# Optimization experiments

Hardware: AMD Instinct MI355X
Metric: run time of the kernel (lower is better)

The kernel has to match this reference:

```python
import jax, jax.numpy as jnp
import numpy as np

EMBED_DIM = 1024
NUM_HEADS = 16
NUM_SIGNALS = 2
B, N = 2, 1024


def taylor_kernel(x):
    # phi(x) = [1, x, (x (outer) x)/sqrt(2)] over the last dim
    d = x.shape[-1]
    x2 = (x[..., :, None] * x[..., None, :]).reshape(*x.shape[:-1], d * d) / 2 ** 0.5
    ones = jnp.ones((*x.shape[:-1], 1), dtype=x.dtype)
    return jnp.concatenate([ones, x, x2], axis=-1)


def setup_inputs() -> dict:
    key = jax.random.key(0)
    ks = jax.random.split(key, 11)
    C = EMBED_DIM
    inp = {
        'query': jax.random.normal(ks[0], (B, N, C), dtype=jnp.float32),
        'key':   jax.random.normal(ks[1], (B, N, C), dtype=jnp.float32),
        'value': jax.random.normal(ks[2], (B, N, C), dtype=jnp.float32),
        'Wq': jax.random.normal(ks[3], (C, C), dtype=jnp.float32) * 0.02,
        'bq': jnp.zeros((C,), dtype=jnp.float32),
        'Wk': jax.random.normal(ks[4], (C, C), dtype=jnp.float32) * 0.02,
        'bk': jnp.zeros((C,), dtype=jnp.float32),
        'Wv': jax.random.normal(ks[5], (C, C), dtype=jnp.float32) * 0.02,
        'bv': jnp.zeros((C,), dtype=jnp.float32),
        'Wo': jax.random.normal(ks[6], (C, C), dtype=jnp.float32) * 0.02,
        'bo': jnp.zeros((C,), dtype=jnp.float32),
    }
    return inp


def reference(query, key, value, Wq, bq, Wk, bk, Wv, bv, Wo, bo):
    Bsz, Nq, C = query.shape
    M = key.shape[1]
    H, S = NUM_HEADS, NUM_SIGNALS
    hd = C // H          # head_dim
    sd = hd // S         # signal_dim
    scale = sd ** -0.5

    q = (query @ Wq.T + bq).reshape(Bsz, Nq, H, S, sd).transpose(0, 2, 3, 1, 4)  # (B,H,S,N,sd)
    k = (key   @ Wk.T + bk).reshape(Bsz, M,  H, S, sd).transpose(0, 2, 3, 1, 4)  # (B,H,S,M,sd)
    v = (value @ Wv.T + bv).reshape(Bsz, M,  H, hd).transpose(0, 2, 1, 3)        # (B,H,M,hd)

    q_phi = taylor_kernel(q * scale)   # (B,H,S,N,F), F = 1+sd+sd^2
    k_phi = taylor_kernel(k)           # (B,H,S,M,F)

    # KV aggregation: O(M * F * hd) per (b,h,s); v broadcast over signal dim
    kv = jnp.einsum('bhsmf,bhmd->bhsfd', k_phi, v)           # (B,H,S,F,hd)
    numer = jnp.einsum('bhsnf,bhsfd->bhsnd', q_phi, kv)      # (B,H,S,N,hd)
    k_sum = k_phi.sum(axis=-2)                               # (B,H,S,F)
    denom = jnp.einsum('bhsnf,bhsf->bhsn', q_phi, k_sum)[..., None]

    out = (numer / (denom + 1e-6)).mean(axis=2)              # avg over signals -> (B,H,N,hd)
    out = out.transpose(0, 2, 1, 3).reshape(Bsz, Nq, C)
    return out @ Wo.T + bo
```

## Files before the change

### kernel.cpp

```cpp
#include <hip/hip_runtime.h>
#include <hip/hip_bf16.h>

#define CC 1024
#define NN 1024
#define BB 2
#define HH 16
#define NT (NN / 64)
#define QSCALE 0.17677669529663687f

typedef short bf16x8 __attribute__((ext_vector_type(8)));
typedef float f32x4  __attribute__((ext_vector_type(4)));
typedef unsigned int u32x2 __attribute__((ext_vector_type(2)));

__device__ __forceinline__ f32x4 mfma16(bf16x8 a, bf16x8 b, f32x4 c) {
    return __builtin_amdgcn_mfma_f32_16x16x32_bf16(a, b, c, 0, 0, 0);
}
__device__ __forceinline__ short f2bf(float x) {
    __hip_bfloat16 h = __float2bfloat16(x);
    return *reinterpret_cast<short*>(&h);
}
__device__ __forceinline__ float bf2f(short s) {
    __hip_bfloat16 h;
    *reinterpret_cast<short*>(&h) = s;
    return __bfloat162float(h);
}
__device__ __forceinline__ int xcd_logical(int hw, int nwg) {
    return (hw & 7) * (nwg >> 3) + (hw >> 3);
}

__global__ __launch_bounds__(256) void qkv_proj(
    const float* __restrict__ xq, const float* __restrict__ xk, const float* __restrict__ xv,
    const float* __restrict__ wq, const float* __restrict__ wk, const float* __restrict__ wv,
    const float* __restrict__ bq, const float* __restrict__ bk, const float* __restrict__ bv,
    short* __restrict__ qt, short* __restrict__ kt, short* __restrict__ vt)
{
    __shared__ short LD[18432];
    short (*A)[72]  = (short(*)[72])LD;
    short (*Bt)[72] = (short(*)[72])(LD + 128 * 72);
    short (*T)[136] = (short(*)[136])LD;

    const int L = xcd_logical(blockIdx.x, 384);
    const int z = L >> 7;
    const int rem = L & 127;
    const int row0 = (rem >> 3) * 128;
    const int col0 = (rem & 7) * 128;

    const int tid  = threadIdx.x;
    const int lane = tid & 63, wave = tid >> 6;
    const int wr = wave >> 1, wc = wave & 1;
    const int l16 = lane & 15, lk = lane >> 4;

    const float* X    = (z == 0) ? xq : (z == 1) ? xk : xv;
    const float* W    = (z == 0) ? wq : (z == 1) ? wk : wv;
    const float* bias = (z == 0) ? bq : (z == 1) ? bk : bv;

    const int str = tid >> 4;
    const int stc = (tid & 15) << 2;

    float4 pa[8], pb[8];
#pragma unroll
    for (int p = 0; p < 8; ++p) {
        pa[p] = *(const float4*)&X[(size_t)(row0 + p * 16 + str) * CC + stc];
        pb[p] = *(const float4*)&W[(size_t)(col0 + p * 16 + str) * CC + stc];
    }

    f32x4 acc[4][4];
#pragma unroll
    for (int i = 0; i < 4; ++i)
#pragma unroll
        for (int j = 0; j < 4; ++j) acc[i][j] = (f32x4){0.f, 0.f, 0.f, 0.f};

    for (int k0 = 0; k0 < CC; k0 += 64) {
#pragma unroll
        for (int p = 0; p < 8; ++p) {
            ushort4 ua = { (unsigned short)f2bf(pa[p].x), (unsigned short)f2bf(pa[p].y),
                           (unsigned short)f2bf(pa[p].z), (unsigned short)f2bf(pa[p].w) };
            *(ushort4*)&A[p * 16 + str][stc] = ua;
            ushort4 ub = { (unsigned short)f2bf(pb[p].x), (unsigned short)f2bf(pb[p].y),
                           (unsigned short)f2bf(pb[p].z), (unsigned short)f2bf(pb[p].w) };
            *(ushort4*)&Bt[p * 16 + str][stc] = ub;
        }
        if (k0 + 64 < CC) {
#pragma unroll
            for (int p = 0; p < 8; ++p) {
                pa[p] = *(const float4*)&X[(size_t)(row0 + p * 16 + str) * CC + k0 + 64 + stc];
                pb[p] = *(const float4*)&W[(size_t)(col0 + p * 16 + str) * CC + k0 + 64 + stc];
            }
        }
        __syncthreads();
#pragma unroll
        for (int ks = 0; ks < 2; ++ks) {
            bf16x8 af[4], bw[4];
#pragma unroll
            for (int i = 0; i < 4; ++i) {
                af[i] = *(const bf16x8*)&A[wr * 64 + i * 16 + l16][ks * 32 + lk * 8];
                bw[i] = *(const bf16x8*)&Bt[wc * 64 + i * 16 + l16][ks * 32 + lk * 8];
            }
#pragma unroll
            for (int mi = 0; mi < 4; ++mi)
#pragma unroll
                for (int nf = 0; nf < 4; ++nf)
                    acc[mi][nf] = mfma16(af[mi], bw[nf], acc[mi][nf]);
        }
        __syncthreads();
    }

    if (z <= 1) {
        short* outp = (z == 0) ? qt : kt;
        const float scl = (z == 0) ? QSCALE : 1.f;
#pragma unroll
        for (int mi = 0; mi < 4; ++mi)
#pragma unroll
            for (int q = 0; q < 4; ++q) {
                const int r = row0 + wr * 64 + mi * 16 + lk * 4 + q;
                const int b = r >> 10, n = r & 1023;
#pragma unroll
                for (int nf = 0; nf < 4; ++nf) {
                    const int o = col0 + wc * 64 + nf * 16 + l16;
                    const int h = o >> 6, s = (o >> 5) & 1, ii = o & 31;
                    float y = (acc[mi][nf][q] + bias[o]) * scl;
                    outp[(((size_t)((b * HH + h) * 2 + s)) << 15) + n * 32 + ii] = f2bf(y);
                }
            }
    } else {
#pragma unroll
        for (int mi = 0; mi < 4; ++mi)
#pragma unroll
            for (int nf = 0; nf < 4; ++nf)
#pragma unroll
                for (int q = 0; q < 4; ++q) {
                    const int c = wc * 64 + nf * 16 + l16;
                    const int r = wr * 64 + mi * 16 + lk * 4 + q;
                    T[c][r] = f2bf(acc[mi][nf][q] + bias[col0 + c]);
                }
        __syncthreads();
        const int b  = row0 >> 10, n0 = row0 & 1023;
        const int c  = tid >> 1, half = tid & 1;
        const int oc = col0 + c, h = oc >> 6, d = oc & 63;
        const size_t base = (((size_t)(b * HH + h)) * 64 + d) * NN + n0 + half * 64;
#pragma unroll
        for (int u = 0; u < 8; ++u)
            *(uint4*)&vt[base + u * 8] = *(const uint4*)&T[c][half * 64 + u * 8];
    }
}

__global__ __launch_bounds__(512) void attn_mfma(
    const short* __restrict__ qt, const short* __restrict__ kt,
    const short* __restrict__ vtg, short* __restrict__ aoh, short* __restrict__ aol)
{
    __shared__ __align__(16) short LDS_[17408];
    short* KsB = LDS_;
    short* VtB = LDS_ + 5120;
    float* OsB = (float*)LDS_;

#define KS(ss, r, c)  KsB[((ss) * 64 + (r)) * 40 + (c)]
#define VT(d, m)      VtB[(d) * 72 + (m)]
#define OS(n, d)      OsB[(n) * 68 + (d)]

    const int L = xcd_logical(blockIdx.x, 256);
    const int bh = L >> 3;
    const int n0 = (L & 7) * 128;

    const int tid  = threadIdx.x;
    const int lane = tid & 63;
    const int wid  = tid >> 6;
    const int s  = wid >> 2;
    const int hq = wid & 3;
    const int l16 = lane & 15, lk = lane >> 4;

    bf16x8 qf[2];
#pragma unroll
    for (int nf = 0; nf < 2; ++nf)
        qf[nf] = *(const bf16x8*)&qt[((size_t)(bh * 2 + s) * NN + n0 + hq * 32 + nf * 16 + l16) * 32 + lk * 8];

    const int kss = tid >> 8, kj = tid & 255, kr = kj >> 2, kc8 = (kj & 3) << 3;
    const int vd = tid >> 3, vc8 = (tid & 7) << 3;

    uint4 kpf, vpf;
    auto load_tiles = [&](int m0) {
        kpf = *(const uint4*)&kt[((size_t)(bh * 2 + kss) * NN + m0 + kr) * 32 + kc8];
        vpf = *(const uint4*)&vtg[((size_t)(bh * 64 + vd)) * NN + m0 + vc8];
    };
    auto commit_tiles = [&]() {
        *(uint4*)&KS(kss, kr, kc8) = kpf;
        *(uint4*)&VT(vd, vc8) = vpf;
    };

    f32x4 accn[2][4];
#pragma unroll
    for (int nf = 0; nf < 2; ++nf)
#pragma unroll
        for (int df = 0; df < 4; ++df) accn[nf][df] = (f32x4){0.f, 0.f, 0.f, 0.f};
    float den[2] = {0.f, 0.f};

    load_tiles(0);

    for (int t = 0; t < NT; ++t) {
        commit_tiles();
        if (t + 1 < NT) load_tiles((t + 1) * 64);
        __syncthreads();

        bf16x8 kf[4], vf[2][4];
#pragma unroll
        for (int mf = 0; mf < 4; ++mf)
            kf[mf] = *(const bf16x8*)&KS(s, mf * 16 + l16, lk * 8);
#pragma unroll
        for (int kb = 0; kb < 2; ++kb)
#pragma unroll
            for (int df = 0; df < 4; ++df)
                vf[kb][df] = *(const bf16x8*)&VT(df * 16 + l16, kb * 32 + lk * 8);

#pragma unroll
        for (int nf = 0; nf < 2; ++nf) {
            unsigned c01[4], c23[4];
#pragma unroll
            for (int mf = 0; mf < 4; ++mf) {
                f32x4 st = mfma16(kf[mf], qf[nf], (f32x4){0.f, 0.f, 0.f, 0.f});
                float p0 = 1.f + st[0] * (1.f + 0.5f * st[0]);
                float p1 = 1.f + st[1] * (1.f + 0.5f * st[1]);
                float p2 = 1.f + st[2] * (1.f + 0.5f * st[2]);
                float p3 = 1.f + st[3] * (1.f + 0.5f * st[3]);
                den[nf] += (p0 + p1) + (p2 + p3);
                asm("v_cvt_pk_bf16_f32 %0, %1, %2" : "=v"(c01[mf]) : "v"(p0), "v"(p1));
                asm("v_cvt_pk_bf16_f32 %0, %1, %2" : "=v"(c23[mf]) : "v"(p2), "v"(p3));
            }
#pragma unroll
            for (int kb = 0; kb < 2; ++kb) {
                u32x2 x0 = __builtin_amdgcn_permlane32_swap(c01[2 * kb], c01[2 * kb + 1], 0, 0);
                u32x2 w02 = __builtin_amdgcn_permlane16_swap(x0.x, x0.y, 0, 0);
                u32x2 x1 = __builtin_amdgcn_permlane32_swap(c23[2 * kb], c23[2 * kb + 1], 0, 0);
                u32x2 w13 = __builtin_amdgcn_permlane16_swap(x1.x, x1.y, 0, 0);
                uint4 u = {w02.x, w13.x, w02.y, w13.y};
                bf16x8 pf = *(bf16x8*)&u;
#pragma unroll
                for (int df = 0; df < 4; ++df)
                    accn[nf][df] = mfma16(pf, vf[kb][df], accn[nf][df]);
            }
        }
        __syncthreads();
    }

    float invq[2][4];
#pragma unroll
    for (int nf = 0; nf < 2; ++nf) {
        float d = den[nf];
        d += __shfl_xor(d, 16, 64);
        d += __shfl_xor(d, 32, 64);
#pragma unroll
        for (int q = 0; q < 4; ++q)
            invq[nf][q] = 0.5f / (__shfl(d, (lane & 48) + lk * 4 + q, 64) + 1e-6f);
    }

    if (s == 0) {
#pragma unroll
        for (int nf = 0; nf < 2; ++nf)
#pragma unroll
            for (int q = 0; q < 4; ++q)
#pragma unroll
                for (int df = 0; df < 4; ++df)
                    OS(hq * 32 + nf * 16 + lk * 4 + q, df * 16 + l16) =
                        accn[nf][df][q] * invq[nf][q];
    }
    __syncthreads();
    if (s == 1) {
        const int b = bh >> 4, h = bh & 15;
#pragma unroll
        for (int nf = 0; nf < 2; ++nf)
#pragma unroll
            for (int q = 0; q < 4; ++q) {
                const int n = hq * 32 + nf * 16 + lk * 4 + q;
#pragma unroll
                for (int df = 0; df < 4; ++df) {
                    const int d = df * 16 + l16;
                    float o = OS(n, d) + accn[nf][df][q] * invq[nf][q];
                    size_t addr = ((size_t)b * NN + n0 + n) * CC + h * 64 + d;
                    short hi = f2bf(o);
                    aoh[addr] = hi;
                    aol[addr] = f2bf(o - bf2f(hi));
                }
            }
    }
#undef KS
#undef VT
#undef OS
}

__global__ __launch_bounds__(256) void wo_proj(
    const short* __restrict__ aoh, const short* __restrict__ aol,
    const float* __restrict__ Wo, const float* __restrict__ bo,
    float* __restrict__ outp)
{
    __shared__ short Ah[64][40], Al[64][40], Wh[64][40], Wl[64][40];

    const int L = xcd_logical(blockIdx.x, 512);
    const int row0 = (L >> 4) * 64;
    const int col0 = (L & 15) * 64;

    const int tid  = threadIdx.x;
    const int lane = tid & 63, wave = tid >> 6;
    const int wr = wave >> 1, wc = wave & 1;
    const int l16 = lane & 15, lk = lane >> 4;

    const int ar  = tid >> 2, ac8 = (tid & 3) << 3;
    const int wrr = tid >> 3, wc4 = (tid & 7) << 2;

    uint4 ph, pl;
    float4 pw[2];
    ph = *(const uint4*)&aoh[(size_t)(row0 + ar) * CC + ac8];
    pl = *(const uint4*)&aol[(size_t)(row0 + ar) * CC + ac8];
#pragma unroll
    for (int p = 0; p < 2; ++p)
        pw[p] = *(const float4*)&Wo[(size_t)(col0 + p * 32 + wrr) * CC + wc4];

    f32x4 acc[2][2];
#pragma unroll
    for (int i = 0; i < 2; ++i)
#pragma unroll
        for (int j = 0; j < 2; ++j) acc[i][j] = (f32x4){0.f, 0.f, 0.f, 0.f};

    for (int k0 = 0; k0 < CC; k0 += 32) {
        *(uint4*)&Ah[ar][ac8] = ph;
        *(uint4*)&Al[ar][ac8] = pl;
#pragma unroll
        for (int p = 0; p < 2; ++p) {
            float v[4] = {pw[p].x, pw[p].y, pw[p].z, pw[p].w};
            unsigned short hs[4], ls[4];
#pragma unroll
            for (int j = 0; j < 4; ++j) {
                short hv = f2bf(v[j]);
                hs[j] = (unsigned short)hv;
                ls[j] = (unsigned short)f2bf(v[j] - bf2f(hv));
            }
            *(ushort4*)&Wh[p * 32 + wrr][wc4] = (ushort4){hs[0], hs[1], hs[2], hs[3]};
            *(ushort4*)&Wl[p * 32 + wrr][wc4] = (ushort4){ls[0], ls[1], ls[2], ls[3]};
        }
        if (k0 + 32 < CC) {
            ph = *(const uint4*)&aoh[(size_t)(row0 + ar) * CC + k0 + 32 + ac8];
            pl = *(const uint4*)&aol[(size_t)(row0 + ar) * CC + k0 + 32 + ac8];
#pragma unroll
            for (int p = 0; p < 2; ++p)
                pw[p] = *(const float4*)&Wo[(size_t)(col0 + p * 32 + wrr) * CC + k0 + 32 + wc4];
        }
        __syncthreads();
        bf16x8 ah[2], al[2], wh[2], wl[2];
#pragma unroll
        for (int i = 0; i < 2; ++i) {
            ah[i] = *(const bf16x8*)&Ah[wr * 32 + i * 16 + l16][lk * 8];
            al[i] = *(const bf16x8*)&Al[wr * 32 + i * 16 + l16][lk * 8];
            wh[i] = *(const bf16x8*)&Wh[wc * 32 + i * 16 + l16][lk * 8];
            wl[i] = *(const bf16x8*)&Wl[wc * 32 + i * 16 + l16][lk * 8];
        }
#pragma unroll
        for (int mi = 0; mi < 2; ++mi)
#pragma unroll
            for (int nj = 0; nj < 2; ++nj) {
                acc[mi][nj] = mfma16(ah[mi], wh[nj], acc[mi][nj]);
                acc[mi][nj] = mfma16(ah[mi], wl[nj], acc[mi][nj]);
                acc[mi][nj] = mfma16(al[mi], wh[nj], acc[mi][nj]);
            }
        __syncthreads();
    }

#pragma unroll
    for (int mi = 0; mi < 2; ++mi)
#pragma unroll
        for (int q = 0; q < 4; ++q) {
            const int r = row0 + wr * 32 + mi * 16 + lk * 4 + q;
#pragma unroll
            for (int nj = 0; nj < 2; ++nj) {
                const int o = col0 + wc * 32 + nj * 16 + l16;
                outp[(size_t)r * CC + o] = acc[mi][nj][q] + bo[o];
            }
        }
}

extern "C" void kernel_launch(void* const* d_in, const int* in_sizes, int n_in,
                              void* d_out, int out_size, void* d_ws, size_t ws_size,
                              hipStream_t stream) {
    const float* query = (const float*)d_in[0];
    const float* key_  = (const float*)d_in[1];
    const float* value = (const float*)d_in[2];
    const float* Wq = (const float*)d_in[3];
    const float* bq = (const float*)d_in[4];
    const float* Wk = (const float*)d_in[5];
    const float* bk = (const float*)d_in[6];
    const float* Wv = (const float*)d_in[7];
    const float* bv = (const float*)d_in[8];
    const float* Wo = (const float*)d_in[9];
    const float* bo = (const float*)d_in[10];
    float* out = (float*)d_out;

    short* qt  = (short*)d_ws;
    short* kt  = qt  + ((size_t)1 << 21);
    short* vt  = kt  + ((size_t)1 << 21);
    short* aoh = vt  + ((size_t)1 << 21);
    short* aol = aoh + ((size_t)1 << 21);

    dim3 blk(256);
    qkv_proj<<<dim3(384), blk, 0, stream>>>(query, key_, value, Wq, Wk, Wv,
                                            bq, bk, bv, qt, kt, vt);
    attn_mfma<<<dim3(256), dim3(512), 0, stream>>>(qt, kt, vt, aoh, aol);
    wo_proj<<<dim3(512), blk, 0, stream>>>(aoh, aol, Wo, bo, out);
}
```

Measured before the change: 83.33 us.

## Pre-convert QKV inputs and weights to bf16 in a separate pass

Adds a cvt_pass kernel that converts the query/key/value activations and the Wq/Wk/Wv weights from fp32 to bf16 in the workspace. The projection GEMM then loads bf16 directly, which halves its global load bytes, drops the per-tile conversion work from the inner loop, and double-buffers two 64-wide K slices held in registers. The cost is an extra kernel launch plus an extra write and read of roughly 36 MB of converted data, so the net gain depends on whether the GEMM was bound by loads or conversion.

```diff
diff --git a/kernel.cpp b/kernel.cpp
--- a/kernel.cpp
+++ b/kernel.cpp
@@ -28,9 +28,34 @@
     return (hw & 7) * (nwg >> 3) + (hw >> 3);
 }
 
-__global__ __launch_bounds__(256) void qkv_proj(
+__global__ __launch_bounds__(256) void cvt_pass(
     const float* __restrict__ xq, const float* __restrict__ xk, const float* __restrict__ xv,
     const float* __restrict__ wq, const float* __restrict__ wk, const float* __restrict__ wv,
+    short* __restrict__ xqb, short* __restrict__ xkb, short* __restrict__ xvb,
+    short* __restrict__ wqb, short* __restrict__ wkb, short* __restrict__ wvb)
+{
+    const int z = blockIdx.z;
+    const float* src = (z == 0) ? xq : (z == 1) ? xk : (z == 2) ? xv :
+                       (z == 3) ? wq : (z == 4) ? wk : wv;
+    short* dst = (z == 0) ? xqb : (z == 1) ? xkb : (z == 2) ? xvb :
+                 (z == 3) ? wqb : (z == 4) ? wkb : wvb;
+    const size_t n = (z < 3) ? ((size_t)1 << 21) : ((size_t)1 << 20);
+
+    for (size_t i = ((size_t)blockIdx.x * 256 + threadIdx.x) * 8; i < n;
+         i += (size_t)gridDim.x * 256 * 8) {
+        float4 v0 = *(const float4*)&src[i];
+        float4 v1 = *(const float4*)&src[i + 4];
+        float v[8] = {v0.x, v0.y, v0.z, v0.w, v1.x, v1.y, v1.z, v1.w};
+        unsigned short h[8];
+#pragma unroll
+        for (int j = 0; j < 8; ++j) h[j] = (unsigned short)f2bf(v[j]);
+        *(uint4*)&dst[i] = *(uint4*)h;
+    }
+}
+
+__global__ __launch_bounds__(256) void qkv_proj(
+    const short* __restrict__ xqb, const short* __restrict__ xkb, const short* __restrict__ xvb,
+    const short* __restrict__ wqb, const short* __restrict__ wkb, const short* __restrict__ wvb,
     const float* __restrict__ bq, const float* __restrict__ bk, const float* __restrict__ bv,
     short* __restrict__ qt, short* __restrict__ kt, short* __restrict__ vt)
 {
@@ -50,18 +75,20 @@
     const int wr = wave >> 1, wc = wave & 1;
     const int l16 = lane & 15, lk = lane >> 4;
 
-    const float* X    = (z == 0) ? xq : (z == 1) ? xk : xv;
-    const float* W    = (z == 0) ? wq : (z == 1) ? wk : wv;
+    const short* X    = (z == 0) ? xqb : (z == 1) ? xkb : xvb;
+    const short* W    = (z == 0) ? wqb : (z == 1) ? wkb : wvb;
     const float* bias = (z == 0) ? bq : (z == 1) ? bk : bv;
 
-    const int str = tid >> 4;
-    const int stc = (tid & 15) << 2;
-
-    float4 pa[8], pb[8];
-#pragma unroll
-    for (int p = 0; p < 8; ++p) {
-        pa[p] = *(const float4*)&X[(size_t)(row0 + p * 16 + str) * CC + stc];
-        pb[p] = *(const float4*)&W[(size_t)(col0 + p * 16 + str) * CC + stc];
+    const int srow = tid >> 3;
+    const int sc8  = (tid & 7) << 3;
+
+    uint4 pa0[4], pb0[4], pa1[4], pb1[4];
+#pragma unroll
+    for (int p = 0; p < 4; ++p) {
+        pa0[p] = *(const uint4*)&X[(size_t)(row0 + p * 32 + srow) * CC + sc8];
+        pb0[p] = *(const uint4*)&W[(size_t)(col0 + p * 32 + srow) * CC + sc8];
+        pa1[p] = *(const uint4*)&X[(size_t)(row0 + p * 32 + srow) * CC + 64 + sc8];
+        pb1[p] = *(const uint4*)&W[(size_t)(col0 + p * 32 + srow) * CC + 64 + sc8];
     }
 
     f32x4 acc[4][4];
@@ -70,21 +97,46 @@
 #pragma unroll
         for (int j = 0; j < 4; ++j) acc[i][j] = (f32x4){0.f, 0.f, 0.f, 0.f};
 
-    for (int k0 = 0; k0 < CC; k0 += 64) {
-#pragma unroll
-        for (int p = 0; p < 8; ++p) {
-            ushort4 ua = { (unsigned short)f2bf(pa[p].x), (unsigned short)f2bf(pa[p].y),
-                           (unsigned short)f2bf(pa[p].z), (unsigned short)f2bf(pa[p].w) };
-            *(ushort4*)&A[p * 16 + str][stc] = ua;
-            ushort4 ub = { (unsigned short)f2bf(pb[p].x), (unsigned short)f2bf(pb[p].y),
-                           (unsigned short)f2bf(pb[p].z), (unsigned short)f2bf(pb[p].w) };
-            *(ushort4*)&Bt[p * 16 + str][stc] = ub;
-        }
-        if (k0 + 64 < CC) {
-#pragma unroll
-            for (int p = 0; p < 8; ++p) {
-                pa[p] = *(const float4*)&X[(size_t)(row0 + p * 16 + str) * CC + k0 + 64 + stc];
-                pb[p] = *(const float4*)&W[(size_t)(col0 + p * 16 + str) * CC + k0 + 64 + stc];
+    for (int k0 = 0; k0 < CC; k0 += 128) {
+#pragma unroll
+        for (int p = 0; p < 4; ++p) {
+            *(uint4*)&A[p * 32 + srow][sc8] = pa0[p];
+            *(uint4*)&Bt[p * 32 + srow][sc8] = pb0[p];
+        }
+        if (k0 + 128 < CC) {
+#pragma unroll
+            for (int p = 0; p < 4; ++p) {
+                pa0[p] = *(const uint4*)&X[(size_t)(row0 + p * 32 + srow) * CC + k0 + 128 + sc8];
+                pb0[p] = *(const uint4*)&W[(size_t)(col0 + p * 32 + srow) * CC + k0 + 128 + sc8];
+            }
+        }
+        __syncthreads();
+#pragma unroll
+        for (int ks = 0; ks < 2; ++ks) {
+            bf16x8 af[4], bw[4];
+#pragma unroll
+            for (int i = 0; i < 4; ++i) {
+                af[i] = *(const bf16x8*)&A[wr * 64 + i * 16 + l16][ks * 32 + lk * 8];
+                bw[i] = *(const bf16x8*)&Bt[wc * 64 + i * 16 + l16][ks * 32 + lk * 8];
+            }
+#pragma unroll
+            for (int mi = 0; mi < 4; ++mi)
+#pragma unroll
+                for (int nf = 0; nf < 4; ++nf)
+                    acc[mi][nf] = mfma16(af[mi], bw[nf], acc[mi][nf]);
+        }
+        __syncthreads();
+
+#pragma unroll
+        for (int p = 0; p < 4; ++p) {
+            *(uint4*)&A[p * 32 + srow][sc8] = pa1[p];
+            *(uint4*)&Bt[p * 32 + srow][sc8] = pb1[p];
+        }
+        if (k0 + 192 < CC) {
+#pragma unroll
+            for (int p = 0; p < 4; ++p) {
+                pa1[p] = *(const uint4*)&X[(size_t)(row0 + p * 32 + srow) * CC + k0 + 192 + sc8];
+                pb1[p] = *(const uint4*)&W[(size_t)(col0 + p * 32 + srow) * CC + k0 + 192 + sc8];
             }
         }
         __syncthreads();
@@ -390,14 +442,25 @@
     const float* bo = (const float*)d_in[10];
     float* out = (float*)d_out;
 
-    short* qt  = (short*)d_ws;
-    short* kt  = qt  + ((size_t)1 << 21);
-    short* vt  = kt  + ((size_t)1 << 21);
-    short* aoh = vt  + ((size_t)1 << 21);
-    short* aol = aoh + ((size_t)1 << 21);
+    short* p = (short*)d_ws;
+    const size_t M2 = (size_t)1 << 21;
+    const size_t M1 = (size_t)1 << 20;
+    short* qt  = p;  p += M2;
+    short* kt  = p;  p += M2;
+    short* vt  = p;  p += M2;
+    short* aoh = p;  p += M2;
+    short* aol = p;  p += M2;
+    short* xqb = p;  p += M2;
+    short* xkb = p;  p += M2;
+    short* xvb = p;  p += M2;
+    short* wqb = p;  p += M1;
+    short* wkb = p;  p += M1;
+    short* wvb = p;  p += M1;
 
     dim3 blk(256);
-    qkv_proj<<<dim3(384), blk, 0, stream>>>(query, key_, value, Wq, Wk, Wv,
+    cvt_pass<<<dim3(128, 1, 6), blk, 0, stream>>>(query, key_, value, Wq, Wk, Wv,
+                                                  xqb, xkb, xvb, wqb, wkb, wvb);
+    qkv_proj<<<dim3(384), blk, 0, stream>>>(xqb, xkb, xvb, wqb, wkb, wvb,
                                             bq, bk, bv, qt, kt, vt);
     attn_mfma<<<dim3(256), dim3(512), 0, stream>>>(qt, kt, vt, aoh, aol);
     wo_proj<<<dim3(512), blk, 0, stream>>>(aoh, aol, Wo, bo, out);
```

Result: slower. 137.0 us (+64.4%).
